# Kernel optimization log

Measured on AMD Instinct MI355X. Metric: run time of the kernel, lower is better.

Reference implementation:

```python
import jax, jax.numpy as jnp
import numpy as np

N, D, H, L = 50000, 128, 4, 3
E = 800000
C = D // H            # head dim = 32
NEG_SLOPE = 0.2       # PyG GATv2Conv default negative_slope
LN_EPS = 1e-5         # nn.LayerNorm default eps


def setup_inputs() -> dict:
    key = jax.random.key(0)
    ks = jax.random.split(key, 8)
    s = 1.0 / np.sqrt(D).astype(np.float32)
    return {
        "fine_poi_x": jax.random.normal(ks[0], (N, D), jnp.float32),
        "edge_index": jax.random.randint(ks[1], (2, E), 0, N, dtype=jnp.int32),
        "Wl": jax.random.normal(ks[2], (L, D, D), jnp.float32) * s,
        "bl": jnp.zeros((L, D), jnp.float32),
        "Wr": jax.random.normal(ks[3], (L, D, D), jnp.float32) * s,
        "br": jnp.zeros((L, D), jnp.float32),
        "att": jax.random.normal(ks[4], (L, H, C), jnp.float32) * s,
        "bias": jnp.zeros((L, D), jnp.float32),
        "gamma": jnp.ones((L, D), jnp.float32),
        "beta": jnp.zeros((L, D), jnp.float32),
    }


def _gatv2_conv(x, src, dst, Wl, bl, Wr, br, att, bias):
    # x: [N, D]; src/dst: [E'] (self-loops already appended)
    xl = (x @ Wl + bl).reshape(N, H, C)   # source-side transform (lin_l)
    xr = (x @ Wr + br).reshape(N, H, C)   # target-side transform (lin_r)
    m = xl[src] + xr[dst]                 # [E', H, C] per-edge pre-activation
    m = jax.nn.leaky_relu(m, NEG_SLOPE)
    e = jnp.einsum("ehc,hc->eh", m, att)  # [E', H] attention logits
    # segment softmax over edges grouped by destination node
    emax = jax.ops.segment_max(e, dst, num_segments=N)      # [N, H]
    ee = jnp.exp(e - emax[dst])
    denom = jax.ops.segment_sum(ee, dst, num_segments=N)    # [N, H]
    alpha = ee / denom[dst]               # self-loops guarantee denom >= 1 term
    out = jax.ops.segment_sum(xl[src] * alpha[:, :, None], dst, num_segments=N)
    return out.reshape(N, D) + bias


def _layernorm(x, g, b):
    mu = jnp.mean(x, axis=-1, keepdims=True)
    var = jnp.var(x, axis=-1, keepdims=True)
    return (x - mu) * jax.lax.rsqrt(var + LN_EPS) * g + b


def reference(fine_poi_x, edge_index, Wl, bl, Wr, br, att, bias, gamma, beta):
    # PyG GATv2Conv add_self_loops=True: append i->i edges
    loops = jnp.arange(N, dtype=edge_index.dtype)
    src = jnp.concatenate([edge_index[0], loops])
    dst = jnp.concatenate([edge_index[1], loops])
    x = fine_poi_x
    for i in range(L):
        h = _gatv2_conv(x, src, dst, Wl[i], bl[i], Wr[i], br[i], att[i], bias[i])
        x = _layernorm(x + h, gamma[i], beta[i])
        if i != L - 1:
            x = jax.nn.relu(x)
    return x
```

## Files before the change

### kernel.cpp

```cpp
#include <hip/hip_runtime.h>

#define N_NODES 50000
#define N_EDGES 800000
#define DIM 128
#define TOT_EDGES (N_EDGES + N_NODES)
#define LOG2E 1.44269504088896f

#define BSHIFT 9
#define BNODES 512
#define NB ((N_NODES + BNODES - 1) / BNODES)
#define BCAP 16384
#define EPB 4096
#define EPT 16
#define NBLK_A ((TOT_EDGES + EPB - 1) / EPB)

typedef __attribute__((ext_vector_type(8))) _Float16 f16x8;
typedef __attribute__((ext_vector_type(2))) _Float16 h2;
typedef __attribute__((ext_vector_type(4))) float f32x4;
typedef decltype(__builtin_amdgcn_cvt_pkrtz(0.f, 0.f)) fp16v2;

__device__ inline uint h2u(h2 v) { return __builtin_bit_cast(uint, v); }
__device__ inline h2 u2h(uint v) { return __builtin_bit_cast(h2, v); }
__device__ inline uint pk2u(fp16v2 v) { return __builtin_bit_cast(uint, v); }

__device__ inline float rowsum16(float v) {
  int x;
  x = __builtin_amdgcn_update_dpp(0, __float_as_int(v), 0x128, 0xF, 0xF, true);
  v += __int_as_float(x);
  x = __builtin_amdgcn_update_dpp(0, __float_as_int(v), 0x124, 0xF, 0xF, true);
  v += __int_as_float(x);
  x = __builtin_amdgcn_update_dpp(0, __float_as_int(v), 0x122, 0xF, 0xF, true);
  v += __int_as_float(x);
  x = __builtin_amdgcn_update_dpp(0, __float_as_int(v), 0x121, 0xF, 0xF, true);
  v += __int_as_float(x);
  return v;
}


__global__ __launch_bounds__(256) void partA_kernel(const int* __restrict__ srcArr,
                                                    const int* __restrict__ dstArr,
                                                    int* __restrict__ bcnt,
                                                    uint2* __restrict__ bbuf) {
  int tid = threadIdx.x;
  int e0 = blockIdx.x * EPB;
  __shared__ int hist[NB], base[NB], loff[NB];
  if (tid < NB) { hist[tid] = 0; loff[tid] = 0; }
  __syncthreads();

  int sv[EPT], dv[EPT];
#pragma unroll
  for (int i = 0; i < EPT; ++i) {
    int e = e0 + i * 256 + tid;
    int s = 0, d = -1;
    if (e < TOT_EDGES) {
      if (e < N_EDGES) { s = srcArr[e]; d = dstArr[e]; }
      else { s = e - N_EDGES; d = s; }
    }
    sv[i] = s; dv[i] = d;
    if (d >= 0) atomicAdd(&hist[d >> BSHIFT], 1);
  }
  __syncthreads();
  if (tid < NB) {
    int h = hist[tid];
    if (h > 0) base[tid] = atomicAdd(&bcnt[tid], h);
  }
  __syncthreads();
#pragma unroll
  for (int i = 0; i < EPT; ++i) {
    int d = dv[i];
    if (d >= 0) {
      int b = d >> BSHIFT;
      int p = atomicAdd(&loff[b], 1);
      bbuf[(size_t)b * BCAP + base[b] + p] = make_uint2((uint)sv[i], (uint)d);
    }
  }
}

__global__ __launch_bounds__(128) void scanb_kernel(const int* __restrict__ bcnt,
                                                    int* __restrict__ colbase,
                                                    int* __restrict__ rowptr) {
  int tid = threadIdx.x;
  int v = (tid < NB) ? bcnt[tid] : 0;
  __shared__ int s[128];
  s[tid] = v;
  __syncthreads();
  for (int off = 1; off < 128; off <<= 1) {
    int t = (tid >= off) ? s[tid - off] : 0;
    __syncthreads();
    s[tid] += t;
    __syncthreads();
  }
  if (tid < NB) colbase[tid] = s[tid] - v;
  if (tid == 0) rowptr[N_NODES] = TOT_EDGES;
}

__global__ __launch_bounds__(512) void partB_kernel(const uint2* __restrict__ bbuf,
                                                    const int* __restrict__ bcnt,
                                                    const int* __restrict__ colbase,
                                                    int* __restrict__ rowptr,
                                                    int* __restrict__ col) {
  int b = blockIdx.x, tid = threadIdx.x;
  int m = bcnt[b];
  int cb = colbase[b];
  const uint2* buf = bbuf + (size_t)b * BCAP;

  __shared__ int cnt[BNODES], scn[BNODES], cur[BNODES];
  cnt[tid] = 0;
  __syncthreads();
  for (int e = tid; e < m; e += 512) {
    int d = (int)buf[e].y;
    atomicAdd(&cnt[d & (BNODES - 1)], 1);
  }
  __syncthreads();
  int c = cnt[tid];
  scn[tid] = c;
  __syncthreads();
  for (int off = 1; off < BNODES; off <<= 1) {
    int t = (tid >= off) ? scn[tid - off] : 0;
    __syncthreads();
    scn[tid] += t;
    __syncthreads();
  }
  int excl = scn[tid] - c;
  int node = b * BNODES + tid;
  if (node < N_NODES) rowptr[node] = cb + excl;
  cur[tid] = excl;
  __syncthreads();
  for (int e = tid; e < m; e += 512) {
    uint2 sd = buf[e];
    int p = atomicAdd(&cur[(int)sd.y & (BNODES - 1)], 1);
    col[cb + p] = (int)sd.x;
  }
}


__global__ __launch_bounds__(256) void convx_kernel(const float* __restrict__ x,
                                                    uint* __restrict__ xb) {
  int t = blockIdx.x * 256 + threadIdx.x;
  if (t < N_NODES * (DIM / 2)) {
    float2 v = ((const float2*)x)[t];
    xb[t] = pk2u(__builtin_amdgcn_cvt_pkrtz(v.x, v.y));
  }
}

__global__ __launch_bounds__(256) void convw_kernel(const float* __restrict__ Wl,
                                                    const float* __restrict__ Wr,
                                                    ushort* __restrict__ Wt) {
  int t = blockIdx.x * 256 + threadIdx.x;
  if (t >= 3 * 2 * DIM * DIM) return;
  int k = t & 127;
  int n = (t >> 7) & 127;
  int w = (t >> 14) & 1;
  int l = t >> 15;
  const float* W = w ? Wr : Wl;
  _Float16 h = (_Float16)W[l * DIM * DIM + k * DIM + n];
  Wt[t] = __builtin_bit_cast(ushort, h);
}

__global__ __launch_bounds__(192) void conva_kernel(const float* __restrict__ att,
                                                    uint* __restrict__ attc) {
  int t = threadIdx.x;
  float a0 = att[2 * t] * LOG2E, a1 = att[2 * t + 1] * LOG2E;
  attc[t] = pk2u(__builtin_amdgcn_cvt_pkrtz(a0, a1));
}


__global__ __launch_bounds__(256) void gemm_mfma_kernel(
    const uint* __restrict__ xb,
    const ushort* __restrict__ Wt,
    const float* __restrict__ bl, const float* __restrict__ br,
    uint* __restrict__ xl, uint* __restrict__ xr) {
  int wave = threadIdx.x >> 6, lane = threadIdx.x & 63;
  int lr = lane & 15, kq = lane >> 4;
  int m0 = blockIdx.x * 64;

  const ushort* W = Wt + (wave >> 1) * (DIM * DIM);
  const float* bias = (wave >> 1) ? br : bl;
  uint* outp = (wave >> 1) ? xr : xl;
  int n0 = (wave & 1) * 64;

  f16x8 bfrag[4][4];
#pragma unroll
  for (int nt = 0; nt < 4; ++nt)
#pragma unroll
    for (int kt = 0; kt < 4; ++kt)
      bfrag[nt][kt] = *(const f16x8*)(W + (n0 + nt * 16 + lr) * DIM + kt * 32 + kq * 8);

  f32x4 acc[4][4];
#pragma unroll
  for (int mt = 0; mt < 4; ++mt)
#pragma unroll
    for (int nt = 0; nt < 4; ++nt)
      acc[mt][nt] = (f32x4){0.f, 0.f, 0.f, 0.f};

#pragma unroll
  for (int mt = 0; mt < 4; ++mt) {
    int m = m0 + mt * 16 + lr;
    int mc = m < N_NODES ? m : N_NODES - 1;
    f16x8 afrag[4];
#pragma unroll
    for (int kt = 0; kt < 4; ++kt)
      afrag[kt] = *(const f16x8*)((const ushort*)xb + (size_t)mc * DIM + kt * 32 + kq * 8);
#pragma unroll
    for (int nt = 0; nt < 4; ++nt)
#pragma unroll
      for (int kt = 0; kt < 4; ++kt)
        acc[mt][nt] = __builtin_amdgcn_mfma_f32_16x16x32_f16(bfrag[nt][kt], afrag[kt],
                                                             acc[mt][nt], 0, 0, 0);
  }

#pragma unroll
  for (int mt = 0; mt < 4; ++mt) {
    int m = m0 + mt * 16 + lr;
    if (m < N_NODES) {
#pragma unroll
      for (int nt = 0; nt < 4; ++nt) {
        int n = n0 + nt * 16 + kq * 4;
        float4 bb = *(const float4*)(bias + n);
        uint2 o;
        o.x = pk2u(__builtin_amdgcn_cvt_pkrtz(acc[mt][nt][0] + bb.x, acc[mt][nt][1] + bb.y));
        o.y = pk2u(__builtin_amdgcn_cvt_pkrtz(acc[mt][nt][2] + bb.z, acc[mt][nt][3] + bb.w));
        *(uint2*)(outp + (size_t)m * (DIM / 2) + (n >> 1)) = o;
      }
    }
  }
}


__global__ __launch_bounds__(64) void att_kernel(
    const uint* __restrict__ xinb, const uint* __restrict__ xlb,
    const uint* __restrict__ xrb, const int* __restrict__ rowptr,
    const int* __restrict__ col, const uint* __restrict__ attc,
    const float* __restrict__ bias, const float* __restrict__ gamma,
    const float* __restrict__ beta, uint* __restrict__ xoutb,
    float* __restrict__ xoutf, int do_relu) {
  int lane = threadIdx.x;
  int n = blockIdx.x;
  size_t rowp = (size_t)n * (DIM / 2) + lane;

  h2 r2 = u2h(xrb[rowp]);
  h2 at2 = u2h(attc[lane]);
  const h2 c02 = {(_Float16)0.2f, (_Float16)0.2f};
  float acc0 = 0.f, acc1 = 0.f, den = 0.f;

  int js = rowptr[n], je = rowptr[n + 1];
  int jm = je - 1;

  int ci = js + lane;
  uint colv = (uint)col[ci < jm ? ci : jm];

  for (int cbase = js; cbase < je; cbase += 64) {
    int cnt = je - cbase;
    if (cnt > 64) cnt = 64;
    int cm = cnt - 1;
    uint colv_next = colv;
    if (cbase + 64 < je) {
      int ci2 = cbase + 64 + lane;
      colv_next = (uint)col[ci2 < jm ? ci2 : jm];
    }

#define GLD(dst, e)                                                          \
  {                                                                          \
    int s_ = __builtin_amdgcn_readlane((int)colv, (e) < cm ? (e) : cm);      \
    dst = xlb[(size_t)s_ * (DIM / 2) + lane];                                \
  }
    uint g0, g1, g2, g3;
    GLD(g0, 0) GLD(g1, 1) GLD(g2, 2) GLD(g3, 3)
    for (int e = 0; e < cnt; e += 4) {
      uint n0_, n1_, n2_, n3_;
      GLD(n0_, e + 4) GLD(n1_, e + 5) GLD(n2_, e + 6) GLD(n3_, e + 7)
#define PROC(i, g)                                                 \
  {                                                                \
    h2 a2 = u2h(g);                                                \
    h2 s2 = a2 + r2;                                               \
    h2 m2 = __builtin_elementwise_max(s2, s2 * c02);               \
    float p = __builtin_amdgcn_fdot2(                              \
        __builtin_bit_cast(fp16v2, m2),                            \
        __builtin_bit_cast(fp16v2, at2), 0.f, false);              \
    p = rowsum16(p);                                               \
    float w = (e + (i) < cnt) ? __builtin_amdgcn_exp2f(p) : 0.f;   \
    den += w;                                                      \
    acc0 = fmaf(w, (float)a2.x, acc0);                             \
    acc1 = fmaf(w, (float)a2.y, acc1);                             \
  }
      PROC(0, g0) PROC(1, g1) PROC(2, g2) PROC(3, g3)
#undef PROC
      g0 = n0_; g1 = n1_; g2 = n2_; g3 = n3_;
    }
#undef GLD
    colv = colv_next;
  }

  float inv = 1.0f / den;
  h2 xi2 = u2h(xinb[rowp]);
  float2 bi = ((const float2*)bias)[lane];
  float o0 = fmaf(acc0, inv, bi.x + (float)xi2.x);
  float o1 = fmaf(acc1, inv, bi.y + (float)xi2.y);

  float s1 = o0 + o1, s2 = o0 * o0 + o1 * o1;
  s1 = rowsum16(s1);
  s2 = rowsum16(s2);
  s1 += __shfl_xor(s1, 16, 64);
  s2 += __shfl_xor(s2, 16, 64);
  s1 += __shfl_xor(s1, 32, 64);
  s2 += __shfl_xor(s2, 32, 64);
  float mean = s1 * (1.0f / DIM);
  float var = s2 * (1.0f / DIM) - mean * mean;
  float rstd = rsqrtf(var + 1e-5f);
  float2 gm = ((const float2*)gamma)[lane];
  float2 bt = ((const float2*)beta)[lane];
  float y0 = (o0 - mean) * rstd * gm.x + bt.x;
  float y1 = (o1 - mean) * rstd * gm.y + bt.y;
  if (do_relu) { y0 = fmaxf(y0, 0.f); y1 = fmaxf(y1, 0.f); }
  if (xoutb) xoutb[rowp] = pk2u(__builtin_amdgcn_cvt_pkrtz(y0, y1));
  if (xoutf) ((float2*)xoutf)[rowp] = make_float2(y0, y1);
}


extern "C" void kernel_launch(void* const* d_in, const int* in_sizes, int n_in,
                              void* d_out, int out_size, void* d_ws, size_t ws_size,
                              hipStream_t stream) {
  const float* x_in  = (const float*)d_in[0];
  const int*   eidx  = (const int*)d_in[1];
  const float* Wl    = (const float*)d_in[2];
  const float* bl    = (const float*)d_in[3];
  const float* Wr    = (const float*)d_in[4];
  const float* br    = (const float*)d_in[5];
  const float* att   = (const float*)d_in[6];
  const float* bias  = (const float*)d_in[7];
  const float* gamma = (const float*)d_in[8];
  const float* beta  = (const float*)d_in[9];
  float* out = (float*)d_out;

  char* p = (char*)d_ws;
  auto alloc = [&](size_t bytes) {
    char* q = p;
    p += (bytes + 255) & ~(size_t)255;
    return q;
  };
  uint*  xb       = (uint*)alloc((size_t)N_NODES * (DIM / 2) * 4);
  uint*  xlb      = (uint*)alloc((size_t)N_NODES * (DIM / 2) * 4);
  uint*  xrb      = (uint*)alloc((size_t)N_NODES * (DIM / 2) * 4);
  ushort* Wt      = (ushort*)alloc((size_t)3 * 2 * DIM * DIM * 2);
  uint*  attc     = (uint*)alloc((size_t)3 * 64 * 4);
  int*   rowptr   = (int*)alloc((size_t)(N_NODES + 1) * 4);
  int*   col      = (int*)alloc((size_t)TOT_EDGES * 4);
  uint2* bbuf     = (uint2*)alloc((size_t)NB * BCAP * 8);
  int*   bcnt     = (int*)alloc((size_t)NB * 4);
  int*   colbase  = (int*)alloc((size_t)NB * 4);

  (void)hipMemsetAsync(bcnt, 0, (size_t)NB * 4, stream);
  partA_kernel<<<NBLK_A, 256, 0, stream>>>(eidx, eidx + N_EDGES, bcnt, bbuf);
  scanb_kernel<<<1, 128, 0, stream>>>(bcnt, colbase, rowptr);
  partB_kernel<<<NB, 512, 0, stream>>>(bbuf, bcnt, colbase, rowptr, col);
  convx_kernel<<<(N_NODES * (DIM / 2) + 255) / 256, 256, 0, stream>>>(x_in, xb);
  convw_kernel<<<(3 * 2 * DIM * DIM + 255) / 256, 256, 0, stream>>>(Wl, Wr, Wt);
  conva_kernel<<<1, 192, 0, stream>>>(att, attc);

  for (int l = 0; l < 3; ++l) {
    gemm_mfma_kernel<<<(N_NODES + 63) / 64, 256, 0, stream>>>(
        xb, Wt + (size_t)l * 2 * DIM * DIM, bl + l * DIM, br + l * DIM, xlb, xrb);
    att_kernel<<<N_NODES, 64, 0, stream>>>(
        xb, xlb, xrb, rowptr, col, attc + l * 64, bias + l * DIM,
        gamma + l * DIM, beta + l * DIM,
        (l == 2) ? nullptr : xb, (l == 2) ? out : nullptr, (l != 2) ? 1 : 0);
  }
}
```

Baseline: 252.1 us.

## Process four edges per wave in attention kernel with 16-byte gathers

Restructures the per-node attention kernel so each wave handles four edges at once: each 16-lane group gathers one source row with uint4 (16-byte) loads and owns 8 features. Head dot products now reduce over 4 lanes with quad DPP instead of 16. Partial accumulators are combined across the groups with shuffles at the end. The goal is wider memory transactions and more gathers in flight per wave. The cost is more accumulator registers, a cross-group reduction, and wasted lanes when a node's degree is not a multiple of four.

After: 251.1 us. No clear change (-0.4%).

```diff
diff --git a/kernel.cpp b/kernel.cpp
--- a/kernel.cpp
+++ b/kernel.cpp
@@ -32,6 +32,15 @@
   x = __builtin_amdgcn_update_dpp(0, __float_as_int(v), 0x122, 0xF, 0xF, true);
   v += __int_as_float(x);
   x = __builtin_amdgcn_update_dpp(0, __float_as_int(v), 0x121, 0xF, 0xF, true);
+  v += __int_as_float(x);
+  return v;
+}
+
+__device__ inline float quadsum4(float v) {
+  int x;
+  x = __builtin_amdgcn_update_dpp(0, __float_as_int(v), 0xB1, 0xF, 0xF, true);
+  v += __int_as_float(x);
+  x = __builtin_amdgcn_update_dpp(0, __float_as_int(v), 0x4E, 0xF, 0xF, true);
   v += __int_as_float(x);
   return v;
 }
@@ -228,92 +237,134 @@
 
 
 __global__ __launch_bounds__(64) void att_kernel(
-    const uint* __restrict__ xinb, const uint* __restrict__ xlb,
-    const uint* __restrict__ xrb, const int* __restrict__ rowptr,
-    const int* __restrict__ col, const uint* __restrict__ attc,
-    const float* __restrict__ bias, const float* __restrict__ gamma,
-    const float* __restrict__ beta, uint* __restrict__ xoutb,
-    float* __restrict__ xoutf, int do_relu) {
+    const uint4* __restrict__ xinb, const uint4* __restrict__ xlb,
+    const uint4* __restrict__ xrb, const int* __restrict__ rowptr,
+    const int* __restrict__ col, const uint4* __restrict__ attc,
+    const float4* __restrict__ bias, const float4* __restrict__ gamma,
+    const float4* __restrict__ beta, uint4* __restrict__ xoutb,
+    float4* __restrict__ xoutf, int do_relu) {
   int lane = threadIdx.x;
+  int j = lane & 15, e4 = lane >> 4;
   int n = blockIdx.x;
-  size_t rowp = (size_t)n * (DIM / 2) + lane;
-
-  h2 r2 = u2h(xrb[rowp]);
-  h2 at2 = u2h(attc[lane]);
+
+  uint4 rq = xrb[n * 16 + j];
+  uint4 aq = attc[j];
+  h2 r2[4] = {u2h(rq.x), u2h(rq.y), u2h(rq.z), u2h(rq.w)};
+  h2 at2[4] = {u2h(aq.x), u2h(aq.y), u2h(aq.z), u2h(aq.w)};
   const h2 c02 = {(_Float16)0.2f, (_Float16)0.2f};
-  float acc0 = 0.f, acc1 = 0.f, den = 0.f;
+
+  float acc[8] = {0.f, 0.f, 0.f, 0.f, 0.f, 0.f, 0.f, 0.f};
+  float den = 0.f;
 
   int js = rowptr[n], je = rowptr[n + 1];
   int jm = je - 1;
 
-  int ci = js + lane;
-  uint colv = (uint)col[ci < jm ? ci : jm];
-
-  for (int cbase = js; cbase < je; cbase += 64) {
-    int cnt = je - cbase;
-    if (cnt > 64) cnt = 64;
-    int cm = cnt - 1;
-    uint colv_next = colv;
-    if (cbase + 64 < je) {
-      int ci2 = cbase + 64 + lane;
-      colv_next = (uint)col[ci2 < jm ? ci2 : jm];
-    }
-
-#define GLD(dst, e)                                                          \
-  {                                                                          \
-    int s_ = __builtin_amdgcn_readlane((int)colv, (e) < cm ? (e) : cm);      \
-    dst = xlb[(size_t)s_ * (DIM / 2) + lane];                                \
-  }
-    uint g0, g1, g2, g3;
-    GLD(g0, 0) GLD(g1, 1) GLD(g2, 2) GLD(g3, 3)
-    for (int e = 0; e < cnt; e += 4) {
-      uint n0_, n1_, n2_, n3_;
-      GLD(n0_, e + 4) GLD(n1_, e + 5) GLD(n2_, e + 6) GLD(n3_, e + 7)
-#define PROC(i, g)                                                 \
-  {                                                                \
-    h2 a2 = u2h(g);                                                \
-    h2 s2 = a2 + r2;                                               \
-    h2 m2 = __builtin_elementwise_max(s2, s2 * c02);               \
-    float p = __builtin_amdgcn_fdot2(                              \
-        __builtin_bit_cast(fp16v2, m2),                            \
-        __builtin_bit_cast(fp16v2, at2), 0.f, false);              \
-    p = rowsum16(p);                                               \
-    float w = (e + (i) < cnt) ? __builtin_amdgcn_exp2f(p) : 0.f;   \
-    den += w;                                                      \
-    acc0 = fmaf(w, (float)a2.x, acc0);                             \
-    acc1 = fmaf(w, (float)a2.y, acc1);                             \
-  }
-      PROC(0, g0) PROC(1, g1) PROC(2, g2) PROC(3, g3)
-#undef PROC
-      g0 = n0_; g1 = n1_; g2 = n2_; g3 = n3_;
-    }
-#undef GLD
-    colv = colv_next;
-  }
+  int ci0 = js + e4;
+  int c_cur = col[ci0 < jm ? ci0 : jm];
+  int ci1 = js + 4 + e4;
+  int c_nxt = col[ci1 < jm ? ci1 : jm];
+  uint4 g_cur = xlb[(size_t)c_cur * 16 + j];
+
+  for (int cbase = js; cbase < je; cbase += 4) {
+    int ci2 = cbase + 8 + e4;
+    int c_n2 = col[ci2 < jm ? ci2 : jm];
+    uint4 g_nxt = xlb[(size_t)c_nxt * 16 + j];
+
+    h2 a0 = u2h(g_cur.x), a1 = u2h(g_cur.y), a2 = u2h(g_cur.z), a3 = u2h(g_cur.w);
+    float p = 0.f;
+    {
+      h2 s0 = a0 + r2[0], s1 = a1 + r2[1], s2 = a2 + r2[2], s3 = a3 + r2[3];
+      h2 m0 = __builtin_elementwise_max(s0, s0 * c02);
+      h2 m1 = __builtin_elementwise_max(s1, s1 * c02);
+      h2 m2 = __builtin_elementwise_max(s2, s2 * c02);
+      h2 m3 = __builtin_elementwise_max(s3, s3 * c02);
+      p = __builtin_amdgcn_fdot2(__builtin_bit_cast(fp16v2, m0),
+                                 __builtin_bit_cast(fp16v2, at2[0]), p, false);
+      p = __builtin_amdgcn_fdot2(__builtin_bit_cast(fp16v2, m1),
+                                 __builtin_bit_cast(fp16v2, at2[1]), p, false);
+      p = __builtin_amdgcn_fdot2(__builtin_bit_cast(fp16v2, m2),
+                                 __builtin_bit_cast(fp16v2, at2[2]), p, false);
+      p = __builtin_amdgcn_fdot2(__builtin_bit_cast(fp16v2, m3),
+                                 __builtin_bit_cast(fp16v2, at2[3]), p, false);
+    }
+    p = quadsum4(p);
+    float w = (cbase + e4 < je) ? __builtin_amdgcn_exp2f(p) : 0.f;
+    den += w;
+    acc[0] = fmaf(w, (float)a0.x, acc[0]);
+    acc[1] = fmaf(w, (float)a0.y, acc[1]);
+    acc[2] = fmaf(w, (float)a1.x, acc[2]);
+    acc[3] = fmaf(w, (float)a1.y, acc[3]);
+    acc[4] = fmaf(w, (float)a2.x, acc[4]);
+    acc[5] = fmaf(w, (float)a2.y, acc[5]);
+    acc[6] = fmaf(w, (float)a3.x, acc[6]);
+    acc[7] = fmaf(w, (float)a3.y, acc[7]);
+
+    g_cur = g_nxt;
+    c_nxt = c_n2;
+  }
+
+#pragma unroll
+  for (int t = 0; t < 8; ++t) {
+    acc[t] += __shfl_xor(acc[t], 16, 64);
+    acc[t] += __shfl_xor(acc[t], 32, 64);
+  }
+  den += __shfl_xor(den, 16, 64);
+  den += __shfl_xor(den, 32, 64);
 
   float inv = 1.0f / den;
-  h2 xi2 = u2h(xinb[rowp]);
-  float2 bi = ((const float2*)bias)[lane];
-  float o0 = fmaf(acc0, inv, bi.x + (float)xi2.x);
-  float o1 = fmaf(acc1, inv, bi.y + (float)xi2.y);
-
-  float s1 = o0 + o1, s2 = o0 * o0 + o1 * o1;
+  uint4 xi4 = xinb[n * 16 + j];
+  h2 xi[4] = {u2h(xi4.x), u2h(xi4.y), u2h(xi4.z), u2h(xi4.w)};
+  float4 b0 = bias[2 * j], b1 = bias[2 * j + 1];
+
+  float o[8];
+  o[0] = fmaf(acc[0], inv, b0.x + (float)xi[0].x);
+  o[1] = fmaf(acc[1], inv, b0.y + (float)xi[0].y);
+  o[2] = fmaf(acc[2], inv, b0.z + (float)xi[1].x);
+  o[3] = fmaf(acc[3], inv, b0.w + (float)xi[1].y);
+  o[4] = fmaf(acc[4], inv, b1.x + (float)xi[2].x);
+  o[5] = fmaf(acc[5], inv, b1.y + (float)xi[2].y);
+  o[6] = fmaf(acc[6], inv, b1.z + (float)xi[3].x);
+  o[7] = fmaf(acc[7], inv, b1.w + (float)xi[3].y);
+
+  float s1 = 0.f, s2 = 0.f;
+#pragma unroll
+  for (int t = 0; t < 8; ++t) { s1 += o[t]; s2 = fmaf(o[t], o[t], s2); }
   s1 = rowsum16(s1);
   s2 = rowsum16(s2);
-  s1 += __shfl_xor(s1, 16, 64);
-  s2 += __shfl_xor(s2, 16, 64);
-  s1 += __shfl_xor(s1, 32, 64);
-  s2 += __shfl_xor(s2, 32, 64);
   float mean = s1 * (1.0f / DIM);
   float var = s2 * (1.0f / DIM) - mean * mean;
   float rstd = rsqrtf(var + 1e-5f);
-  float2 gm = ((const float2*)gamma)[lane];
-  float2 bt = ((const float2*)beta)[lane];
-  float y0 = (o0 - mean) * rstd * gm.x + bt.x;
-  float y1 = (o1 - mean) * rstd * gm.y + bt.y;
-  if (do_relu) { y0 = fmaxf(y0, 0.f); y1 = fmaxf(y1, 0.f); }
-  if (xoutb) xoutb[rowp] = pk2u(__builtin_amdgcn_cvt_pkrtz(y0, y1));
-  if (xoutf) ((float2*)xoutf)[rowp] = make_float2(y0, y1);
+
+  float4 g0 = gamma[2 * j], g1 = gamma[2 * j + 1];
+  float4 t0 = beta[2 * j], t1 = beta[2 * j + 1];
+  float y[8];
+  y[0] = (o[0] - mean) * rstd * g0.x + t0.x;
+  y[1] = (o[1] - mean) * rstd * g0.y + t0.y;
+  y[2] = (o[2] - mean) * rstd * g0.z + t0.z;
+  y[3] = (o[3] - mean) * rstd * g0.w + t0.w;
+  y[4] = (o[4] - mean) * rstd * g1.x + t1.x;
+  y[5] = (o[5] - mean) * rstd * g1.y + t1.y;
+  y[6] = (o[6] - mean) * rstd * g1.z + t1.z;
+  y[7] = (o[7] - mean) * rstd * g1.w + t1.w;
+  if (do_relu) {
+#pragma unroll
+    for (int t = 0; t < 8; ++t) y[t] = fmaxf(y[t], 0.f);
+  }
+
+  if (e4 == 0) {
+    if (xoutb) {
+      uint4 ov;
+      ov.x = pk2u(__builtin_amdgcn_cvt_pkrtz(y[0], y[1]));
+      ov.y = pk2u(__builtin_amdgcn_cvt_pkrtz(y[2], y[3]));
+      ov.z = pk2u(__builtin_amdgcn_cvt_pkrtz(y[4], y[5]));
+      ov.w = pk2u(__builtin_amdgcn_cvt_pkrtz(y[6], y[7]));
+      xoutb[n * 16 + j] = ov;
+    }
+    if (xoutf) {
+      xoutf[n * 32 + 2 * j] = make_float4(y[0], y[1], y[2], y[3]);
+      xoutf[n * 32 + 2 * j + 1] = make_float4(y[4], y[5], y[6], y[7]);
+    }
+  }
 }
 
 
@@ -361,8 +412,10 @@
     gemm_mfma_kernel<<<(N_NODES + 63) / 64, 256, 0, stream>>>(
         xb, Wt + (size_t)l * 2 * DIM * DIM, bl + l * DIM, br + l * DIM, xlb, xrb);
     att_kernel<<<N_NODES, 64, 0, stream>>>(
-        xb, xlb, xrb, rowptr, col, attc + l * 64, bias + l * DIM,
-        gamma + l * DIM, beta + l * DIM,
-        (l == 2) ? nullptr : xb, (l == 2) ? out : nullptr, (l != 2) ? 1 : 0);
-  }
-}
+        (const uint4*)xb, (const uint4*)xlb, (const uint4*)xrb, rowptr, col,
+        (const uint4*)(attc + l * 64), (const float4*)(bias + l * DIM),
+        (const float4*)(gamma + l * DIM), (const float4*)(beta + l * DIM),
+        (l == 2) ? nullptr : (uint4*)xb, (l == 2) ? (float4*)out : nullptr,
+        (l != 2) ? 1 : 0);
+  }
+}
```
